# Kernel tuning notes

Hardware: AMD Instinct MI355X
Metric: run time of the kernel (lower is better)

The kernel has to match this reference:

```python
import jax, jax.numpy as jnp
import numpy as np

NEG_INF = -1e10  # matches the -10000000000.0 additive mask in the torch source


def setup_inputs() -> dict:
    key = jax.random.key(0)
    k1, k2, k3, k4 = jax.random.split(key, 4)
    bs, h, S, d = 4, 16, 2048, 64
    bs_h = bs * h
    query = jax.random.normal(k1, (bs_h, S, d), dtype=jnp.float32)
    key_t = jax.random.normal(k2, (bs_h, S, d), dtype=jnp.float32)
    value = jax.random.normal(k3, (bs_h, S, d), dtype=jnp.float32)
    attn_mask = jax.random.randint(k4, (bs, S), 0, 2).astype(jnp.int32)
    return {"query": query, "key": key_t, "value": value,
            "attn_mask": attn_mask, "decod_mask": 1}


def reference(query, key, value, attn_mask, decod_mask):
    bs_h, K, d_k = key.shape
    Q = query.shape[1]
    bs = attn_mask.shape[0]
    h = bs_h // bs

    # scores: [bs_h, Q, K]
    scores = jnp.einsum('bqd,bkd->bqk', query, key) / jnp.sqrt(
        jnp.asarray(d_k, dtype=query.dtype))

    # padding mask: positions where attn_mask == 0 get -1e10.
    # torch repeats the [bs, Q, K] mask h times along the batch axis
    # (order: [mask; mask; ...]), i.e. batch index b in bs_h maps to b % bs.
    pad = (attn_mask == 0).astype(scores.dtype) * NEG_INF  # [bs, K]
    scores = (scores.reshape(h, bs, Q, K) + pad[None, :, None, :]).reshape(bs_h, Q, K)

    if decod_mask is not None:
        causal = jnp.triu(jnp.full((Q, K), NEG_INF, dtype=scores.dtype), k=1)
        scores = scores + causal[None, :, :]

    attn = jax.nn.softmax(scores, axis=-1)
    # dropout p=0.0 -> identity
    return jnp.einsum('bqk,bkd->bqd', attn, value)
```

## Files before the change

kernel.cpp:

```cpp
#include <hip/hip_runtime.h>
#include <hip/hip_bf16.h>

#define S_LEN 2048
#define DH 64
#define NBATCH 4
#define LOG2E 1.44269504088896f
#define SCL2E 0.18033688011112042f
#define PADC  (-1.44269504088896e10f)
#define NEG_BIG -1e10f
#define NEG_CAUSAL -3.0e38f

typedef __attribute__((ext_vector_type(8))) short short8;
typedef __attribute__((ext_vector_type(4))) float floatx4;
typedef __attribute__((ext_vector_type(4))) unsigned uintx4;

__device__ inline float fast_exp2(float x) {
#if __has_builtin(__builtin_amdgcn_exp2f)
  return __builtin_amdgcn_exp2f(x);
#else
  return exp2f(x);
#endif
}

__device__ inline short f2bf(float x) {
  union { float f; unsigned u; } v; v.f = x;
  unsigned r = v.u + 0x7fffu + ((v.u >> 16) & 1u);
  return (short)(r >> 16);
}

__device__ inline short8 pack8(float4 a, float4 b) {
  short8 r;
  r[0] = f2bf(a.x); r[1] = f2bf(a.y); r[2] = f2bf(a.z); r[3] = f2bf(a.w);
  r[4] = f2bf(b.x); r[5] = f2bf(b.y); r[6] = f2bf(b.z); r[7] = f2bf(b.w);
  return r;
}

__device__ inline unsigned packhi(unsigned hi, unsigned lo) {
#if __has_builtin(__builtin_amdgcn_perm)
  return __builtin_amdgcn_perm(hi, lo, 0x07060302u);
#else
  return (hi & 0xFFFF0000u) | (lo >> 16);
#endif
}

#define MFMA32(a, b, c) __builtin_amdgcn_mfma_f32_16x16x32_bf16(a, b, c, 0, 0, 0)

__global__ void prep_aux(const int* __restrict__ maskg, unsigned* __restrict__ sums,
                         unsigned long long* __restrict__ mb) {
  const int i = blockIdx.x * 256 + (int)threadIdx.x;
  if (i < 4096) sums[i] = 0u;
  if (blockIdx.x == 16) {
    const int t = (int)threadIdx.x;
    if (t < 128) {
      const int b = t >> 5, kt = t & 31;
      const int* mp = &maskg[b * S_LEN + kt * 64];
      unsigned long long m = 0ull;
#pragma unroll
      for (int j = 0; j < 64; j += 4) {
        int4 v = *(const int4*)&mp[j];
        unsigned nib = (v.x ? 1u : 0u) | (v.y ? 2u : 0u) | (v.z ? 4u : 0u) | (v.w ? 8u : 0u);
        m |= (unsigned long long)nib << j;
      }
      mb[t] = m;
    }
  }
}

__global__ void prep_kv(const float* __restrict__ Kg, const float* __restrict__ Vg,
                        short8* __restrict__ Kf, short8* __restrict__ Vf,
                        const int* __restrict__ maskg, float* __restrict__ sums) {
  const int gid = (int)blockIdx.x;
  if (gid < 4096) {
    const int idx = gid * 256 + (int)threadIdx.x;
    const int lane = idx & 63;
    const int t = idx >> 6;
    const int nt = t & 3, ks = (t >> 2) & 1;
    const int kt = (t >> 3) & 31;
    const int bh = t >> 8;
    const int c = lane & 15, g = lane >> 4;
    const float* src = Kg + ((size_t)bh * S_LEN + kt * 64 + nt * 16 + c) * DH + ks * 32 + g * 8;
    float4 a = *(const float4*)src;
    float4 b = *(const float4*)(src + 4);
    Kf[idx] = pack8(a, b);
  } else {
    const int idx = (gid - 4096) * 256 + (int)threadIdx.x;
    const int lane = idx & 63;
    const int t = idx >> 6;
    const int dt = t & 3, nt2 = (t >> 2) & 1;
    const int kt = (t >> 3) & 31;
    const int bh = t >> 8;
    const int b = bh & (NBATCH - 1);
    const int c = lane & 15, g = lane >> 4;
    const int key0 = kt * 64 + nt2 * 32 + g * 4;
    const float* src = Vg + ((size_t)bh * S_LEN + key0) * DH + dt * 16 + c;
    int4 m0 = *(const int4*)&maskg[b * S_LEN + key0];
    int4 m1 = *(const int4*)&maskg[b * S_LEN + key0 + 16];
    short8 r;
    float s = 0.f;
    {
      float v0 = src[(size_t)0 * DH], v1 = src[(size_t)1 * DH];
      float v2 = src[(size_t)2 * DH], v3 = src[(size_t)3 * DH];
      r[0] = f2bf(v0); r[1] = f2bf(v1); r[2] = f2bf(v2); r[3] = f2bf(v3);
      s += (m0.x ? v0 : 0.f) + (m0.y ? v1 : 0.f) + (m0.z ? v2 : 0.f) + (m0.w ? v3 : 0.f);
    }
    {
      float v0 = src[(size_t)16 * DH], v1 = src[(size_t)17 * DH];
      float v2 = src[(size_t)18 * DH], v3 = src[(size_t)19 * DH];
      r[4] = f2bf(v0); r[5] = f2bf(v1); r[6] = f2bf(v2); r[7] = f2bf(v3);
      s += (m1.x ? v0 : 0.f) + (m1.y ? v1 : 0.f) + (m1.z ? v2 : 0.f) + (m1.w ? v3 : 0.f);
    }
    Vf[idx] = r;
    s += __shfl_xor(s, 16);
    s += __shfl_xor(s, 32);
    if (lane < 16) atomicAdd(&sums[bh * 64 + dt * 16 + lane], s);
  }
}

__device__ __forceinline__ void loadk(const short8* __restrict__ kbase, int kt,
                                      int lane, short8 (&dst)[8]) {
  const short8* p = kbase + ((size_t)kt * 8) * 64 + lane;
#pragma unroll
  for (int i = 0; i < 8; ++i) dst[i] = p[i * 64];
}

__device__ __forceinline__ void loadv(const short8* __restrict__ vbase, int kt,
                                      int lane, short8 (&dst)[8]) {
  const short8* p = vbase + ((size_t)kt * 8) * 64 + lane;
#pragma unroll
  for (int i = 0; i < 8; ++i) dst[i] = p[i * 64];
}

__device__ __forceinline__ void compute_tile(
    int kt, int qbase, int c, int g,
    const short8 (&kf)[8], unsigned long long mb, const short8 (&vf)[8],
    const short8 (&qf)[2][2], const short8& ones,
    floatx4 (&acc)[2][4], floatx4 (&acc_l)[2])
{
  const unsigned long long sh = mb >> (g * 4);
  const unsigned mlo = (unsigned)sh, mhi = (unsigned)(sh >> 32);
  floatx4 padv[4];
#pragma unroll
  for (int r = 0; r < 4; ++r) {
    padv[0][r] = ((mlo >> r) & 1u)        ? 0.f : PADC;
    padv[1][r] = ((mlo >> (16 + r)) & 1u) ? 0.f : PADC;
    padv[2][r] = ((mhi >> r) & 1u)        ? 0.f : PADC;
    padv[3][r] = ((mhi >> (16 + r)) & 1u) ? 0.f : PADC;
  }

#pragma unroll
  for (int s2 = 0; s2 < 2; ++s2) {
    if (kt * 64 > qbase + s2 * 16 + 15) continue;
    floatx4 st[4];
    __builtin_amdgcn_s_setprio(1);
#pragma unroll
    for (int nt = 0; nt < 4; ++nt) {
      floatx4 cc = (floatx4){0.f, 0.f, 0.f, 0.f};
      cc = MFMA32(kf[nt],     qf[s2][0], cc);
      cc = MFMA32(kf[4 + nt], qf[s2][1], cc);
      st[nt] = cc;
    }
    __builtin_amdgcn_s_setprio(0);
    const int q = qbase + s2 * 16 + c;
    const bool causal = (kt * 64 + 63) > (qbase + s2 * 16);
    unsigned pu[4][4];
#pragma unroll
    for (int nt = 0; nt < 4; ++nt) {
#pragma unroll
      for (int r = 0; r < 4; ++r) {
        float arg = fmaf(st[nt][r], SCL2E, padv[nt][r]);
        if (causal) {
          const int key = kt * 64 + nt * 16 + g * 4 + r;
          arg = (key > q) ? NEG_CAUSAL : arg;
        }
        pu[nt][r] = __float_as_uint(fast_exp2(arg)) + 0x8000u;
      }
    }
    short8 pP[2];
#pragma unroll
    for (int nt2 = 0; nt2 < 2; ++nt2) {
      uintx4 wv;
      wv[0] = packhi(pu[2 * nt2][1],     pu[2 * nt2][0]);
      wv[1] = packhi(pu[2 * nt2][3],     pu[2 * nt2][2]);
      wv[2] = packhi(pu[2 * nt2 + 1][1], pu[2 * nt2 + 1][0]);
      wv[3] = packhi(pu[2 * nt2 + 1][3], pu[2 * nt2 + 1][2]);
      pP[nt2] = __builtin_bit_cast(short8, wv);
    }
    __builtin_amdgcn_s_setprio(1);
#pragma unroll
    for (int nt2 = 0; nt2 < 2; ++nt2) {
      acc_l[s2] = MFMA32(pP[nt2], ones, acc_l[s2]);
#pragma unroll
      for (int dt = 0; dt < 4; ++dt)
        acc[s2][dt] = MFMA32(pP[nt2], vf[nt2 * 4 + dt], acc[s2][dt]);
    }
    __builtin_amdgcn_s_setprio(0);
  }
}

__global__ __launch_bounds__(256, 2) void flash_fwd7(
    const float* __restrict__ Qg,
    const unsigned long long* __restrict__ mbArr,
    const short8* __restrict__ KfB, const short8* __restrict__ VfB,
    float* __restrict__ Og)
{
  const int bh = blockIdx.x;
  const int b  = bh & (NBATCH - 1);
  const int tid = (int)threadIdx.x;
  const int w = tid >> 6, lane = tid & 63;
  const int widx = (int)blockIdx.y * 4 + w;
  const int c = lane & 15, g = lane >> 4;

  const short8 ones = {0x3F80, 0x3F80, 0x3F80, 0x3F80, 0x3F80, 0x3F80, 0x3F80, 0x3F80};
  const short8* kbase = KfB + (size_t)bh * 32 * 8 * 64;
  const short8* vbase = VfB + (size_t)bh * 32 * 8 * 64;

#pragma unroll
  for (int half = 0; half < 2; ++half) {
    const int ch = half ? (63 - widx) : widx;
    const int qbase = ch * 32;
    const int ktmax = ch >> 1;

    short8 qf[2][2];
#pragma unroll
    for (int s2 = 0; s2 < 2; ++s2) {
      const float* qp = Qg + ((size_t)bh * S_LEN + qbase + s2 * 16 + c) * DH + g * 8;
#pragma unroll
      for (int ks = 0; ks < 2; ++ks) {
        float4 a  = *(const float4*)(qp + ks * 32);
        float4 b4 = *(const float4*)(qp + ks * 32 + 4);
        qf[s2][ks] = pack8(a, b4);
      }
    }

    floatx4 acc[2][4];
    floatx4 acc_l[2];
#pragma unroll
    for (int s2 = 0; s2 < 2; ++s2) {
      acc_l[s2] = (floatx4){0.f, 0.f, 0.f, 0.f};
#pragma unroll
      for (int dt = 0; dt < 4; ++dt) acc[s2][dt] = (floatx4){0.f, 0.f, 0.f, 0.f};
    }

    short8 kfA[8], kfB_[8];
    unsigned long long mbA = mbArr[(b << 5)];
    unsigned long long mbB = 0ull;
    loadk(kbase, 0, lane, kfA);
    for (int kt = 0; kt <= ktmax; kt += 2) {
      const bool hasB = (kt + 1 <= ktmax);
      {
        short8 vf[8];
        loadv(vbase, kt, lane, vf);
        if (hasB) {
          loadk(kbase, kt + 1, lane, kfB_);
          mbB = mbArr[(b << 5) | (kt + 1)];
        }
        compute_tile(kt, qbase, c, g, kfA, mbA, vf, qf, ones, acc, acc_l);
      }
      if (hasB) {
        short8 vf[8];
        loadv(vbase, kt + 1, lane, vf);
        if (kt + 2 <= ktmax) {
          loadk(kbase, kt + 2, lane, kfA);
          mbA = mbArr[(b << 5) | (kt + 2)];
        }
        compute_tile(kt + 1, qbase, c, g, kfB_, mbB, vf, qf, ones, acc, acc_l);
      }
    }

#pragma unroll
    for (int s2 = 0; s2 < 2; ++s2) {
      float rr[4];
#pragma unroll
      for (int r = 0; r < 4; ++r) rr[r] = 1.f / acc_l[s2][r];
#pragma unroll
      for (int dt = 0; dt < 4; ++dt)
#pragma unroll
        for (int r = 0; r < 4; ++r)
          Og[((size_t)bh * S_LEN + qbase + s2 * 16 + g * 4 + r) * DH + dt * 16 + c] =
              acc[s2][dt][r] * rr[r];
    }
  }
}

__global__ void fixup_write(const float* __restrict__ Vg, const int* __restrict__ maskg,
                            const float* __restrict__ sums, float* __restrict__ Og)
{
  const int bh = blockIdx.x;
  const int b  = bh & (NBATCH - 1);
  const int d  = (int)threadIdx.x;
  int fmin = S_LEN, n = 0;
  for (int k = d; k < S_LEN; k += 64) {
    if (maskg[b * S_LEN + k] != 0) { ++n; if (k < fmin) fmin = k; }
  }
#pragma unroll
  for (int off = 1; off < 64; off <<= 1) {
    fmin = min(fmin, __shfl_xor(fmin, off));
    n += __shfl_xor(n, off);
  }
  if (fmin == 0) return;
  const float ms = sums[bh * 64 + d];
  float pre = 0.f;
  for (int q = 0; q < fmin; ++q) {
    pre += Vg[((size_t)bh * S_LEN + q) * DH + d];
    Og[((size_t)bh * S_LEN + q) * DH + d] = (pre + ms) / (float)(q + 1 + n);
  }
}

__global__ __launch_bounds__(256, 2) void flash_fwd_lds(
    const float* __restrict__ Qg, const float* __restrict__ Kg,
    const float* __restrict__ Vg, const int* __restrict__ maskg,
    float* __restrict__ Og)
{
  const int qt  = blockIdx.x;
  const int bh  = blockIdx.y;
  const int b   = bh & (NBATCH - 1);
  const int tid = (int)threadIdx.x;
  const int w = tid >> 6, lane = tid & 63;
  const int g = lane >> 4, c = lane & 15;

  __shared__ __align__(16) short Ks[64 * 72];
  __shared__ __align__(16) short Vt[64 * 72];
  __shared__ __align__(16) short Ps[4][32 * 72];

  short8 qf[2][2];
#pragma unroll
  for (int s2 = 0; s2 < 2; ++s2) {
    const float* qp = Qg + ((size_t)bh * S_LEN + qt * 128 + w * 32 + s2 * 16 + c) * DH + g * 8;
#pragma unroll
    for (int ks = 0; ks < 2; ++ks) {
      float4 a  = *(const float4*)(qp + ks * 32);
      float4 bq = *(const float4*)(qp + ks * 32 + 4);
      qf[s2][ks] = pack8(a, bq);
    }
  }

  floatx4 acc[2][4];
  float mrow[2][4], lrow[2][4];
#pragma unroll
  for (int s2 = 0; s2 < 2; ++s2) {
#pragma unroll
    for (int i = 0; i < 4; ++i) acc[s2][i] = (floatx4){0.f, 0.f, 0.f, 0.f};
#pragma unroll
    for (int r = 0; r < 4; ++r) { mrow[s2][r] = -3.4e38f; lrow[s2][r] = 0.f; }
  }

  const int rstage = tid >> 2;
  const int dstage = (tid & 3) * 16;
  const int ktmax = 2 * qt + 1;

  for (int kt = 0; kt <= ktmax; ++kt) {
    __syncthreads();
    {
      const size_t rowbase = ((size_t)bh * S_LEN + kt * 64 + rstage) * DH + dstage;
      const float* kp = Kg + rowbase;
      const float* vp = Vg + rowbase;
      float4 k0 = *(const float4*)kp;       float4 k1 = *(const float4*)(kp + 4);
      float4 k2 = *(const float4*)(kp + 8); float4 k3 = *(const float4*)(kp + 12);
      *(short8*)&Ks[rstage * 72 + dstage]     = pack8(k0, k1);
      *(short8*)&Ks[rstage * 72 + dstage + 8] = pack8(k2, k3);
      float4 v0 = *(const float4*)vp;       float4 v1 = *(const float4*)(vp + 4);
      float4 v2 = *(const float4*)(vp + 8); float4 v3 = *(const float4*)(vp + 12);
      float vv[16] = {v0.x, v0.y, v0.z, v0.w, v1.x, v1.y, v1.z, v1.w,
                      v2.x, v2.y, v2.z, v2.w, v3.x, v3.y, v3.z, v3.w};
#pragma unroll
      for (int i = 0; i < 16; ++i) Vt[(dstage + i) * 72 + rstage] = f2bf(vv[i]);
    }
    __syncthreads();

    float padv[4];
#pragma unroll
    for (int nt = 0; nt < 4; ++nt)
      padv[nt] = (maskg[b * S_LEN + kt * 64 + nt * 16 + c] != 0) ? 0.f : NEG_BIG;

    short8 kf[2][4];
#pragma unroll
    for (int ks = 0; ks < 2; ++ks)
#pragma unroll
      for (int nt = 0; nt < 4; ++nt)
        kf[ks][nt] = *(const short8*)&Ks[(nt * 16 + c) * 72 + ks * 32 + g * 8];

    bool act[2];
#pragma unroll
    for (int s2 = 0; s2 < 2; ++s2)
      act[s2] = (kt * 64) <= (qt * 128 + w * 32 + s2 * 16 + 15);

#pragma unroll
    for (int s2 = 0; s2 < 2; ++s2) {
      if (!act[s2]) continue;
      floatx4 sv[4];
#pragma unroll
      for (int nt = 0; nt < 4; ++nt) {
        floatx4 cc = (floatx4){0.f, 0.f, 0.f, 0.f};
        cc = MFMA32(qf[s2][0], kf[0][nt], cc);
        cc = MFMA32(qf[s2][1], kf[1][nt], cc);
        sv[nt] = cc;
      }
      const int qrow0 = qt * 128 + w * 32 + s2 * 16 + g * 4;
#pragma unroll
      for (int nt = 0; nt < 4; ++nt) {
        const int key = kt * 64 + nt * 16 + c;
#pragma unroll
        for (int r = 0; r < 4; ++r) {
          float s = sv[nt][r] * 0.125f + padv[nt];
          if (key > qrow0 + r) s = NEG_CAUSAL;
          sv[nt][r] = s;
        }
      }
#pragma unroll
      for (int r = 0; r < 4; ++r) {
        float mx = fmaxf(fmaxf(sv[0][r], sv[1][r]), fmaxf(sv[2][r], sv[3][r]));
        mx = fmaxf(mx, __shfl_xor(mx, 1));
        mx = fmaxf(mx, __shfl_xor(mx, 2));
        mx = fmaxf(mx, __shfl_xor(mx, 4));
        mx = fmaxf(mx, __shfl_xor(mx, 8));
        const float mold = mrow[s2][r];
        const float mnew = fmaxf(mold, mx);
        const float corr = fast_exp2((mold - mnew) * LOG2E);
        float ps = 0.f;
#pragma unroll
        for (int nt = 0; nt < 4; ++nt) {
          float p = fast_exp2((sv[nt][r] - mnew) * LOG2E);
          sv[nt][r] = p;
          ps += p;
        }
        ps += __shfl_xor(ps, 1);
        ps += __shfl_xor(ps, 2);
        ps += __shfl_xor(ps, 4);
        ps += __shfl_xor(ps, 8);
        lrow[s2][r] = lrow[s2][r] * corr + ps;
        mrow[s2][r] = mnew;
#pragma unroll
        for (int dt = 0; dt < 4; ++dt) acc[s2][dt][r] *= corr;
      }
#pragma unroll
      for (int nt = 0; nt < 4; ++nt)
#pragma unroll
        for (int r = 0; r < 4; ++r)
          Ps[w][(s2 * 16 + g * 4 + r) * 72 + nt * 16 + c] = f2bf(sv[nt][r]);
    }

#pragma unroll
    for (int ks = 0; ks < 2; ++ks) {
      short8 pf0 = {}, pf1 = {};
      if (act[0]) pf0 = *(const short8*)&Ps[w][c * 72 + ks * 32 + g * 8];
      if (act[1]) pf1 = *(const short8*)&Ps[w][(16 + c) * 72 + ks * 32 + g * 8];
#pragma unroll
      for (int dt = 0; dt < 4; ++dt) {
        short8 vfr = *(const short8*)&Vt[(dt * 16 + c) * 72 + ks * 32 + g * 8];
        if (act[0]) acc[0][dt] = MFMA32(pf0, vfr, acc[0][dt]);
        if (act[1]) acc[1][dt] = MFMA32(pf1, vfr, acc[1][dt]);
      }
    }
  }

#pragma unroll
  for (int s2 = 0; s2 < 2; ++s2) {
    float rl[4];
#pragma unroll
    for (int r = 0; r < 4; ++r) rl[r] = 1.f / lrow[s2][r];
    const size_t obase = ((size_t)bh * S_LEN + qt * 128 + w * 32 + s2 * 16 + g * 4) * DH + c;
#pragma unroll
    for (int dt = 0; dt < 4; ++dt)
#pragma unroll
      for (int r = 0; r < 4; ++r)
        Og[obase + (size_t)r * DH + dt * 16] = acc[s2][dt][r] * rl[r];
  }
}

__global__ void fixup(const float* __restrict__ Vg, const int* __restrict__ maskg,
                      float* __restrict__ Og)
{
  const int bh = blockIdx.x;
  const int b  = bh & (NBATCH - 1);
  const int tid = (int)threadIdx.x;
  __shared__ int sFirst;
  __shared__ float4 sRed[64][16];
  __shared__ int sCnt[64];
  if (tid == 0) sFirst = S_LEN;
  __syncthreads();
  for (int k = tid; k < S_LEN; k += 1024)
    if (maskg[b * S_LEN + k] != 0) atomicMin(&sFirst, k);
  __syncthreads();
  const int f = sFirst;
  if (f == 0) return;

  const int dq = tid & 15, kg = tid >> 4;
  float4 a = {0.f, 0.f, 0.f, 0.f}; int cnt = 0;
  for (int k = kg; k < S_LEN; k += 64) {
    if (maskg[b * S_LEN + k] != 0) {
      float4 v = *(const float4*)&Vg[((size_t)bh * S_LEN + k) * DH + dq * 4];
      a.x += v.x; a.y += v.y; a.z += v.z; a.w += v.w; cnt++;
    }
  }
  sRed[kg][dq] = a;
  if (dq == 0) sCnt[kg] = cnt;
  __syncthreads();
  if (tid < 64) {
    const int q4 = tid >> 2, e = tid & 3;
    float ms = 0.f; int n = 0;
#pragma unroll 4
    for (int i = 0; i < 64; ++i) {
      const float* p4 = (const float*)&sRed[i][q4];
      ms += p4[e];
      n += sCnt[i];
    }
    float pre = 0.f;
    for (int q = 0; q < f; ++q) {
      pre += Vg[((size_t)bh * S_LEN + q) * DH + tid];
      Og[((size_t)bh * S_LEN + q) * DH + tid] = (pre + ms) / (float)(q + 1 + n);
    }
  }
}

extern "C" void kernel_launch(void* const* d_in, const int* in_sizes, int n_in,
                              void* d_out, int out_size, void* d_ws, size_t ws_size,
                              hipStream_t stream) {
  const float* Q = (const float*)d_in[0];
  const float* K = (const float*)d_in[1];
  const float* V = (const float*)d_in[2];
  const int* mask = (const int*)d_in[3];
  float* O = (float*)d_out;

  const size_t KF_BYTES = (size_t)64 * S_LEN * DH * 2;
  const size_t SUM_BYTES = (size_t)4096 * sizeof(float);
  const size_t MB_BYTES  = (size_t)128 * sizeof(unsigned long long);
  if (ws_size >= 2 * KF_BYTES + SUM_BYTES + MB_BYTES) {
    short8* Kf = (short8*)d_ws;
    short8* Vf = (short8*)((char*)d_ws + KF_BYTES);
    float* sums = (float*)((char*)d_ws + 2 * KF_BYTES);
    unsigned long long* mbArr =
        (unsigned long long*)((char*)d_ws + 2 * KF_BYTES + SUM_BYTES);
    prep_aux<<<dim3(17), dim3(256), 0, stream>>>(mask, (unsigned*)sums, mbArr);
    prep_kv<<<dim3(8192), dim3(256), 0, stream>>>(K, V, Kf, Vf, mask, sums);
    flash_fwd7<<<dim3(64, 8), dim3(256), 0, stream>>>(Q, mbArr, Kf, Vf, O);
    fixup_write<<<dim3(64), dim3(64), 0, stream>>>(V, mask, sums, O);
  } else {
    flash_fwd_lds<<<dim3(16, 64), dim3(256), 0, stream>>>(Q, K, V, mask, O);
    fixup<<<dim3(64), dim3(1024), 0, stream>>>(V, mask, O);
  }
}
```

Baseline: 210.6 us.

## Restage K/V bf16 repack through LDS with coalesced loads and fewer atomics

Rewrites the K/V preprocessing kernel so each block loads a contiguous 64x64 tile of K and V with float4 reads, converts it to bf16 in LDS, and then emits the MFMA fragment layout from shared memory. The masked V column sums are reduced in LDS before one atomic per column per tile, replacing many strided scalar V loads and per-wavefront atomics. Mask first-index and count computation moves into the aux kernel, so the fixup kernel no longer rescans the mask, and the sums buffer is zeroed with a memset. The cost is more LDS use and a block barrier, plus an extra memset launch.

```diff
diff --git a/kernel.cpp b/kernel.cpp
--- a/kernel.cpp
+++ b/kernel.cpp
@@ -35,6 +35,10 @@
   return r;
 }
 
+__device__ inline float4 scale4(float4 v, float m) {
+  return make_float4(v.x * m, v.y * m, v.z * m, v.w * m);
+}
+
 __device__ inline unsigned packhi(unsigned hi, unsigned lo) {
 #if __has_builtin(__builtin_amdgcn_perm)
   return __builtin_amdgcn_perm(hi, lo, 0x07060302u);
@@ -45,74 +49,117 @@
 
 #define MFMA32(a, b, c) __builtin_amdgcn_mfma_f32_16x16x32_bf16(a, b, c, 0, 0, 0)
 
-__global__ void prep_aux(const int* __restrict__ maskg, unsigned* __restrict__ sums,
-                         unsigned long long* __restrict__ mb) {
-  const int i = blockIdx.x * 256 + (int)threadIdx.x;
-  if (i < 4096) sums[i] = 0u;
-  if (blockIdx.x == 16) {
-    const int t = (int)threadIdx.x;
-    if (t < 128) {
-      const int b = t >> 5, kt = t & 31;
-      const int* mp = &maskg[b * S_LEN + kt * 64];
-      unsigned long long m = 0ull;
-#pragma unroll
-      for (int j = 0; j < 64; j += 4) {
-        int4 v = *(const int4*)&mp[j];
-        unsigned nib = (v.x ? 1u : 0u) | (v.y ? 2u : 0u) | (v.z ? 4u : 0u) | (v.w ? 8u : 0u);
-        m |= (unsigned long long)nib << j;
-      }
-      mb[t] = m;
-    }
-  }
-}
-
-__global__ void prep_kv(const float* __restrict__ Kg, const float* __restrict__ Vg,
-                        short8* __restrict__ Kf, short8* __restrict__ Vf,
-                        const int* __restrict__ maskg, float* __restrict__ sums) {
-  const int gid = (int)blockIdx.x;
-  if (gid < 4096) {
-    const int idx = gid * 256 + (int)threadIdx.x;
-    const int lane = idx & 63;
-    const int t = idx >> 6;
-    const int nt = t & 3, ks = (t >> 2) & 1;
-    const int kt = (t >> 3) & 31;
-    const int bh = t >> 8;
-    const int c = lane & 15, g = lane >> 4;
-    const float* src = Kg + ((size_t)bh * S_LEN + kt * 64 + nt * 16 + c) * DH + ks * 32 + g * 8;
-    float4 a = *(const float4*)src;
-    float4 b = *(const float4*)(src + 4);
-    Kf[idx] = pack8(a, b);
-  } else {
-    const int idx = (gid - 4096) * 256 + (int)threadIdx.x;
-    const int lane = idx & 63;
-    const int t = idx >> 6;
-    const int dt = t & 3, nt2 = (t >> 2) & 1;
-    const int kt = (t >> 3) & 31;
-    const int bh = t >> 8;
-    const int b = bh & (NBATCH - 1);
-    const int c = lane & 15, g = lane >> 4;
-    const int key0 = kt * 64 + nt2 * 32 + g * 4;
-    const float* src = Vg + ((size_t)bh * S_LEN + key0) * DH + dt * 16 + c;
-    int4 m0 = *(const int4*)&maskg[b * S_LEN + key0];
-    int4 m1 = *(const int4*)&maskg[b * S_LEN + key0 + 16];
+__global__ void prep_aux2(const int* __restrict__ maskg,
+                          unsigned long long* __restrict__ mb,
+                          int* __restrict__ fn)
+{
+  const int b = (int)blockIdx.x;
+  const int tid = (int)threadIdx.x;
+  __shared__ int sF[4], sN[4];
+
+  if (tid < 32) {
+    const int* mp = &maskg[b * S_LEN + tid * 64];
+    unsigned long long m = 0ull;
+#pragma unroll
+    for (int j = 0; j < 64; j += 4) {
+      int4 v = *(const int4*)&mp[j];
+      unsigned nib = (v.x ? 1u : 0u) | (v.y ? 2u : 0u) | (v.z ? 4u : 0u) | (v.w ? 8u : 0u);
+      m |= (unsigned long long)nib << j;
+    }
+    mb[b * 32 + tid] = m;
+  }
+
+  int fmin = S_LEN, n = 0;
+  for (int k = tid; k < S_LEN; k += 256)
+    if (maskg[b * S_LEN + k] != 0) { ++n; if (k < fmin) fmin = k; }
+#pragma unroll
+  for (int off = 1; off < 64; off <<= 1) {
+    fmin = min(fmin, __shfl_xor(fmin, off));
+    n += __shfl_xor(n, off);
+  }
+  const int w = tid >> 6;
+  if ((tid & 63) == 0) { sF[w] = fmin; sN[w] = n; }
+  __syncthreads();
+  if (tid == 0) {
+    int F = sF[0], N = sN[0];
+#pragma unroll
+    for (int i = 1; i < 4; ++i) { F = min(F, sF[i]); N += sN[i]; }
+    fn[b * 2] = F; fn[b * 2 + 1] = N;
+  }
+}
+
+#define KT_STRIDE 72
+#define SR_STRIDE 68
+
+__global__ __launch_bounds__(256, 2) void prep_kv2(
+    const float* __restrict__ Kg, const float* __restrict__ Vg,
+    const int* __restrict__ maskg,
+    short8* __restrict__ Kf, short8* __restrict__ Vf,
+    float* __restrict__ sums)
+{
+  const int blk = (int)blockIdx.x;
+  const int bh = blk >> 5, kt = blk & 31;
+  const int b = bh & (NBATCH - 1);
+  const int tid = (int)threadIdx.x;
+  const int row = tid >> 2, seg = tid & 3;
+
+  __shared__ __align__(16) short Kt[64 * KT_STRIDE];
+  __shared__ __align__(16) short Vt[64 * KT_STRIDE];
+  __shared__ __align__(16) float sredf[64 * SR_STRIDE];
+
+  const size_t gbase = ((size_t)bh * S_LEN + kt * 64 + row) * DH + seg * 16;
+  {
+    float4 a0 = *(const float4*)(Kg + gbase);
+    float4 a1 = *(const float4*)(Kg + gbase + 4);
+    float4 a2 = *(const float4*)(Kg + gbase + 8);
+    float4 a3 = *(const float4*)(Kg + gbase + 12);
+    *(short8*)&Kt[row * KT_STRIDE + seg * 16]     = pack8(a0, a1);
+    *(short8*)&Kt[row * KT_STRIDE + seg * 16 + 8] = pack8(a2, a3);
+  }
+  {
+    float4 a0 = *(const float4*)(Vg + gbase);
+    float4 a1 = *(const float4*)(Vg + gbase + 4);
+    float4 a2 = *(const float4*)(Vg + gbase + 8);
+    float4 a3 = *(const float4*)(Vg + gbase + 12);
+    *(short8*)&Vt[row * KT_STRIDE + seg * 16]     = pack8(a0, a1);
+    *(short8*)&Vt[row * KT_STRIDE + seg * 16 + 8] = pack8(a2, a3);
+    const float mf = (maskg[b * S_LEN + kt * 64 + row] != 0) ? 1.f : 0.f;
+    float* sr = &sredf[row * SR_STRIDE + seg * 16];
+    *(float4*)(sr + 0)  = scale4(a0, mf);
+    *(float4*)(sr + 4)  = scale4(a1, mf);
+    *(float4*)(sr + 8)  = scale4(a2, mf);
+    *(float4*)(sr + 12) = scale4(a3, mf);
+  }
+  __syncthreads();
+
+  const int w = tid >> 6, lane = tid & 63;
+  const int c = lane & 15, g = lane >> 4;
+  const size_t obase = (size_t)(bh * 32 + kt) * 8;
+
+#pragma unroll
+  for (int i = 0; i < 2; ++i) {
+    const int q = 2 * w + i;
+    const int ks = q >> 2, nt = q & 3;
+    short8 v = *(const short8*)&Kt[(nt * 16 + c) * KT_STRIDE + ks * 32 + g * 8];
+    Kf[(obase + q) * 64 + lane] = v;
+  }
+#pragma unroll
+  for (int i = 0; i < 2; ++i) {
+    const int q = 2 * w + i;
+    const int nt2 = q >> 2, dt = q & 3;
     short8 r;
-    float s = 0.f;
-    {
-      float v0 = src[(size_t)0 * DH], v1 = src[(size_t)1 * DH];
-      float v2 = src[(size_t)2 * DH], v3 = src[(size_t)3 * DH];
-      r[0] = f2bf(v0); r[1] = f2bf(v1); r[2] = f2bf(v2); r[3] = f2bf(v3);
-      s += (m0.x ? v0 : 0.f) + (m0.y ? v1 : 0.f) + (m0.z ? v2 : 0.f) + (m0.w ? v3 : 0.f);
-    }
-    {
-      float v0 = src[(size_t)16 * DH], v1 = src[(size_t)17 * DH];
-      float v2 = src[(size_t)18 * DH], v3 = src[(size_t)19 * DH];
-      r[4] = f2bf(v0); r[5] = f2bf(v1); r[6] = f2bf(v2); r[7] = f2bf(v3);
-      s += (m1.x ? v0 : 0.f) + (m1.y ? v1 : 0.f) + (m1.z ? v2 : 0.f) + (m1.w ? v3 : 0.f);
-    }
-    Vf[idx] = r;
-    s += __shfl_xor(s, 16);
-    s += __shfl_xor(s, 32);
-    if (lane < 16) atomicAdd(&sums[bh * 64 + dt * 16 + lane], s);
+#pragma unroll
+    for (int j = 0; j < 8; ++j) {
+      const int key = nt2 * 32 + ((j >= 4) ? 16 : 0) + g * 4 + (j & 3);
+      r[j] = Vt[key * KT_STRIDE + dt * 16 + c];
+    }
+    Vf[(obase + q) * 64 + lane] = r;
+  }
+  if (tid < 64) {
+    float a = 0.f;
+#pragma unroll 8
+    for (int r2 = 0; r2 < 64; ++r2) a += sredf[r2 * SR_STRIDE + tid];
+    atomicAdd(&sums[bh * 64 + tid], a);
   }
 }
 
@@ -282,25 +329,17 @@
   }
 }
 
-__global__ void fixup_write(const float* __restrict__ Vg, const int* __restrict__ maskg,
-                            const float* __restrict__ sums, float* __restrict__ Og)
+__global__ void fixup_write2(const float* __restrict__ Vg, const int* __restrict__ fn,
+                             const float* __restrict__ sums, float* __restrict__ Og)
 {
   const int bh = blockIdx.x;
   const int b  = bh & (NBATCH - 1);
   const int d  = (int)threadIdx.x;
-  int fmin = S_LEN, n = 0;
-  for (int k = d; k < S_LEN; k += 64) {
-    if (maskg[b * S_LEN + k] != 0) { ++n; if (k < fmin) fmin = k; }
-  }
-#pragma unroll
-  for (int off = 1; off < 64; off <<= 1) {
-    fmin = min(fmin, __shfl_xor(fmin, off));
-    n += __shfl_xor(n, off);
-  }
-  if (fmin == 0) return;
+  const int f  = fn[b * 2], n = fn[b * 2 + 1];
+  if (f == 0) return;
   const float ms = sums[bh * 64 + d];
   float pre = 0.f;
-  for (int q = 0; q < fmin; ++q) {
+  for (int q = 0; q < f; ++q) {
     pre += Vg[((size_t)bh * S_LEN + q) * DH + d];
     Og[((size_t)bh * S_LEN + q) * DH + d] = (pre + ms) / (float)(q + 1 + n);
   }
@@ -521,19 +560,22 @@
   const int* mask = (const int*)d_in[3];
   float* O = (float*)d_out;
 
-  const size_t KF_BYTES = (size_t)64 * S_LEN * DH * 2;
+  const size_t KF_BYTES  = (size_t)64 * S_LEN * DH * 2;
   const size_t SUM_BYTES = (size_t)4096 * sizeof(float);
   const size_t MB_BYTES  = (size_t)128 * sizeof(unsigned long long);
-  if (ws_size >= 2 * KF_BYTES + SUM_BYTES + MB_BYTES) {
+  const size_t FN_BYTES  = (size_t)8 * sizeof(int);
+  if (ws_size >= 2 * KF_BYTES + SUM_BYTES + MB_BYTES + FN_BYTES) {
     short8* Kf = (short8*)d_ws;
     short8* Vf = (short8*)((char*)d_ws + KF_BYTES);
     float* sums = (float*)((char*)d_ws + 2 * KF_BYTES);
     unsigned long long* mbArr =
         (unsigned long long*)((char*)d_ws + 2 * KF_BYTES + SUM_BYTES);
-    prep_aux<<<dim3(17), dim3(256), 0, stream>>>(mask, (unsigned*)sums, mbArr);
-    prep_kv<<<dim3(8192), dim3(256), 0, stream>>>(K, V, Kf, Vf, mask, sums);
+    int* fn = (int*)((char*)d_ws + 2 * KF_BYTES + SUM_BYTES + MB_BYTES);
+    hipMemsetAsync(sums, 0, SUM_BYTES, stream);
+    prep_aux2<<<dim3(4), dim3(256), 0, stream>>>(mask, mbArr, fn);
+    prep_kv2<<<dim3(2048), dim3(256), 0, stream>>>(K, V, mask, Kf, Vf, sums);
     flash_fwd7<<<dim3(64, 8), dim3(256), 0, stream>>>(Q, mbArr, Kf, Vf, O);
-    fixup_write<<<dim3(64), dim3(64), 0, stream>>>(V, mask, sums, O);
+    fixup_write2<<<dim3(64), dim3(64), 0, stream>>>(V, fn, sums, O);
   } else {
     flash_fwd_lds<<<dim3(16, 64), dim3(256), 0, stream>>>(Q, K, V, mask, O);
     fixup<<<dim3(64), dim3(1024), 0, stream>>>(V, mask, O);
```

New measurement: 203.7 us. 1.03x faster.
